# Optimization experiments

Hardware: AMD Instinct MI355X
Metric: run time of the kernel (lower is better)

## Reference

```python
import jax, jax.numpy as jnp
import numpy as np
import math

B, N, C = 8, 2048, 512

def setup_inputs() -> dict:
    key = jax.random.key(0)
    ks = jax.random.split(key, 7)
    s = 1.0 / math.sqrt(C)
    return {
        "feature": jax.random.normal(ks[0], (B, N, C), dtype=jnp.float32),
        "wq": jax.random.uniform(ks[1], (C, C), jnp.float32, -s, s),
        "bq": jax.random.uniform(ks[2], (C,), jnp.float32, -s, s),
        "wk": jax.random.uniform(ks[3], (C, C), jnp.float32, -s, s),
        "bk": jax.random.uniform(ks[4], (C,), jnp.float32, -s, s),
        "wv": jax.random.uniform(ks[5], (C, C), jnp.float32, -s, s),
        "bv": jax.random.uniform(ks[6], (C,), jnp.float32, -s, s),
    }

def reference(feature, wq, bq, wk, bk, wv, bv):
    # torch nn.Linear: x @ W.T + b
    q = jnp.einsum('bnc,dc->bnd', feature, wq) + bq
    k = jnp.einsum('bnc,dc->bnd', feature, wk) + bk
    v = jnp.einsum('bnc,dc->bnd', feature, wv) + bv
    scores = jnp.einsum('bnd,bmd->bnm', q, k)          # [B, N, N]
    attn = jax.nn.softmax(scores, axis=2) / math.sqrt(C)  # post-softmax scale (as in source)
    v_star = jnp.einsum('bnm,bmd->bnd', attn, v)
    return feature + v_star
```

## Files before the change

### kernel.cpp

```cpp
#include <hip/hip_runtime.h>
#include <cstdint>
#include <cstddef>


typedef __bf16 bf16x8 __attribute__((ext_vector_type(8)));
typedef float f32x4 __attribute__((ext_vector_type(4)));
typedef short short4v __attribute__((ext_vector_type(4)));

__device__ __forceinline__ short f2b(float f) {
  union { float f; unsigned u; } u; u.f = f;
  unsigned r = (u.u + 0x7fffu + ((u.u >> 16) & 1u)) >> 16;
  return (short)r;
}

#define GLDS(gptr, lptr) \
  __builtin_amdgcn_global_load_lds( \
      (const __attribute__((address_space(1))) unsigned int*)(const void*)(gptr), \
      (__attribute__((address_space(3))) unsigned int*)(void*)(lptr), 16, 0, 0)

__device__ __forceinline__ bf16x8 ldfrag64(const short* buf, int row, int kq) {
  return *(const bf16x8*)(buf + row * 64 + ((kq ^ (row & 7)) * 8));
}

template <int VM>
__device__ __forceinline__ void ph_mid() {
  if constexpr (VM >= 0) asm volatile("s_waitcnt vmcnt(%0)" ::"n"(VM) : "memory");
  __builtin_amdgcn_s_barrier();
  __builtin_amdgcn_s_setprio(1);
}
__device__ __forceinline__ void ph_end() {
  __builtin_amdgcn_s_setprio(0);
  __builtin_amdgcn_s_barrier();
  __builtin_amdgcn_sched_barrier(0);
}

__device__ __forceinline__ void ldA4(bf16x8 (&a)[4][2], const short* buf, int rb, int l4) {
#pragma unroll
  for (int j = 0; j < 4; ++j)
#pragma unroll
    for (int kk = 0; kk < 2; ++kk) a[j][kk] = ldfrag64(buf, rb + j * 16, kk * 4 + l4);
}
__device__ __forceinline__ void ld2(bf16x8 (&b)[2][2], const short* buf, int rb, int l4) {
#pragma unroll
  for (int n = 0; n < 2; ++n)
#pragma unroll
    for (int kk = 0; kk < 2; ++kk) b[n][kk] = ldfrag64(buf, rb + n * 16, kk * 4 + l4);
}
__device__ __forceinline__ void mm42(f32x4 (&acc)[8][4], const bf16x8 (&a)[4][2],
                                     const bf16x8 (&b)[2][2], int io, int no) {
#pragma unroll
  for (int j = 0; j < 4; ++j)
#pragma unroll
    for (int n = 0; n < 2; ++n)
#pragma unroll
      for (int kk = 0; kk < 2; ++kk)
        acc[io + j][no + n] = __builtin_amdgcn_mfma_f32_16x16x32_bf16(
            a[j][kk], b[n][kk], acc[io + j][no + n], 0, 0, 0);
}
__device__ __forceinline__ void mm22(f32x4 (&acc)[4][4], const bf16x8 (&a)[2][2],
                                     const bf16x8 (&b)[2][2], int io, int no) {
#pragma unroll
  for (int j = 0; j < 2; ++j)
#pragma unroll
    for (int n = 0; n < 2; ++n)
#pragma unroll
      for (int kk = 0; kk < 2; ++kk)
        acc[io + j][no + n] = __builtin_amdgcn_mfma_f32_16x16x32_bf16(
            a[j][kk], b[n][kk], acc[io + j][no + n], 0, 0, 0);
}

__global__ __launch_bounds__(256) void prep(const float* __restrict__ f,
                                            const float* __restrict__ w0,
                                            const float* __restrict__ w1,
                                            const float* __restrict__ w2,
                                            const float* __restrict__ b0,
                                            const float* __restrict__ b1,
                                            const float* __restrict__ b2,
                                            short* __restrict__ Xb, short* __restrict__ Wb,
                                            float* __restrict__ biasP, float* __restrict__ l) {
  const int bid = blockIdx.x;
  const int t = threadIdx.x;
  if (bid < 8192) {
    int i = bid * 256 + t;
    float4 v = ((const float4*)f)[i];
    short4v o = { f2b(v.x), f2b(v.y), f2b(v.z), f2b(v.w) };
    *(short4v*)(Xb + (size_t)i * 4) = o;
  } else if (bid < 8960) {
    int i = (bid - 8192) * 256 + t;
    const float* src = (i < 65536) ? w0 : (i < 131072) ? w1 : w2;
    float4 v = ((const float4*)src)[i & 65535];
    short4v o = { f2b(v.x), f2b(v.y), f2b(v.z), f2b(v.w) };
    *(short4v*)(Wb + (size_t)i * 4) = o;
  } else {
    int i = (bid - 8960) * 256 + t;
    float4 z = { 0.f, 0.f, 0.f, 0.f };
    ((float4*)l)[i * 2] = z;
    ((float4*)l)[i * 2 + 1] = z;
    if (i < 1536) {
      const float* s = (i < 512) ? b0 : (i < 1024) ? b1 : b2;
      biasP[i] = s[i & 511];
    }
  }
}

__global__ __launch_bounds__(256) void gemm_qkv(const short* __restrict__ X,
                                                const short* __restrict__ Wall,
                                                const float* __restrict__ biasP,
                                                short* __restrict__ Out,
                                                short* __restrict__ VtOut) {
  __shared__ __align__(16) short Xs[128 * 64];
  __shared__ __align__(16) short Ws[128 * 64];
  const int z = blockIdx.z;
  const short* Wm = Wall + (size_t)z * 262144;
  const int m0 = blockIdx.y * 128, n0 = blockIdx.x * 128;
  const int t = threadIdx.x;
  const int lane = t & 63, w = t >> 6;
  const int wn = (w & 1) * 64, wm = (w >> 1) * 64;
  const int fr = lane & 15, l4 = lane >> 4;

  f32x4 acc[4][4] = {};

  for (int k0 = 0; k0 < 512; k0 += 64) {
    __syncthreads();
#pragma unroll
    for (int u = 0; u < 4; ++u) {
      int cc = t + u * 256;
      int r = cc >> 3, cs = cc & 7;
      int kk = ((cs ^ (r & 7)) * 8);
      GLDS(X + (size_t)(m0 + r) * 512 + k0 + kk, Xs + cc * 8);
      GLDS(Wm + (size_t)(n0 + r) * 512 + k0 + kk, Ws + cc * 8);
    }
    __syncthreads();
#pragma unroll
    for (int h = 0; h < 2; ++h) {
      bf16x8 wf[4], xf[4];
#pragma unroll
      for (int i = 0; i < 4; ++i) wf[i] = ldfrag64(Ws, wn + i * 16 + fr, h * 4 + l4);
#pragma unroll
      for (int j = 0; j < 4; ++j) xf[j] = ldfrag64(Xs, wm + j * 16 + fr, h * 4 + l4);
      if (z < 2) {
#pragma unroll
        for (int i = 0; i < 4; ++i)
#pragma unroll
          for (int j = 0; j < 4; ++j)
            acc[i][j] = __builtin_amdgcn_mfma_f32_16x16x32_bf16(wf[i], xf[j], acc[i][j], 0, 0, 0);
      } else {
#pragma unroll
        for (int i = 0; i < 4; ++i)
#pragma unroll
          for (int j = 0; j < 4; ++j)
            acc[i][j] = __builtin_amdgcn_mfma_f32_16x16x32_bf16(xf[i], wf[j], acc[i][j], 0, 0, 0);
      }
    }
  }

  const int rq = l4 * 4;
  if (z < 2) {
#pragma unroll
    for (int i = 0; i < 4; ++i) {
      int nb = n0 + wn + i * 16 + rq;
      float4 bs = *(const float4*)(biasP + z * 512 + nb);
#pragma unroll
      for (int j = 0; j < 4; ++j) {
        int m = m0 + wm + j * 16 + fr;
        short4v o = { f2b(acc[i][j][0] + bs.x), f2b(acc[i][j][1] + bs.y),
                      f2b(acc[i][j][2] + bs.z), f2b(acc[i][j][3] + bs.w) };
        *(short4v*)(Out + (size_t)z * 8388608 + (size_t)m * 512 + nb) = o;
      }
    }
  } else {
    const int zB = blockIdx.y >> 4;
    const int mb = m0 & 2047;
#pragma unroll
    for (int j = 0; j < 4; ++j) {
      int d = n0 + wn + j * 16 + fr;
      float bd = biasP[1024 + d];
#pragma unroll
      for (int i = 0; i < 4; ++i) {
        int mloc = mb + wm + i * 16 + rq;
        short4v o = { f2b(acc[i][j][0] + bd), f2b(acc[i][j][1] + bd),
                      f2b(acc[i][j][2] + bd), f2b(acc[i][j][3] + bd) };
        *(short4v*)(VtOut + (size_t)zB * 1048576 + (size_t)d * 2048 + mloc) = o;
      }
    }
  }
}

__global__ __launch_bounds__(512, 2) void gemm_qk8(const short* __restrict__ Q,
                                                   const short* __restrict__ Kb,
                                                   short* __restrict__ P,
                                                   float* __restrict__ l) {
  __shared__ __align__(16) short As[2][16384];
  __shared__ __align__(16) short Bs[2][16384];
  const int z = blockIdx.z;
  const short* __restrict__ A = Kb + (size_t)z * 1048576;
  const short* __restrict__ B = Q + (size_t)z * 1048576;
  const int m0 = blockIdx.y * 256;
  const int n0 = blockIdx.x * 256;
  const int t = threadIdx.x;
  const int lane = t & 63, w = t >> 6;
  const int aw = (w >> 2) * 64, bw = (w & 3) * 32;
  const int fr = lane & 15, l4 = lane >> 4;
  const int r0 = t >> 3;
  const int kswz = ((t & 7) ^ (r0 & 7)) * 8;
  const short* pA = A + (size_t)(m0 + r0) * 512 + kswz;
  const short* pB = B + (size_t)(n0 + r0) * 512 + kswz;

#define QK_STG_A(buf, h, kt) do { \
    GLDS(pA + (size_t)((h) * 128) * 512 + (kt) * 64, &As[(buf)][(h) * 8192 + t * 8]); \
    GLDS(pA + (size_t)((h) * 128 + 64) * 512 + (kt) * 64, &As[(buf)][(h) * 8192 + 4096 + t * 8]); \
  } while (0)
#define QK_STG_B(buf, h, kt) do { \
    GLDS(pB + (size_t)((h) * 128) * 512 + (kt) * 64, &Bs[(buf)][(h) * 8192 + t * 8]); \
    GLDS(pB + (size_t)((h) * 128 + 64) * 512 + (kt) * 64, &Bs[(buf)][(h) * 8192 + 4096 + t * 8]); \
  } while (0)

  f32x4 acc[8][4] = {};

  QK_STG_A(0, 0, 0); QK_STG_B(0, 0, 0); QK_STG_B(0, 1, 0); QK_STG_A(0, 1, 0);
  QK_STG_A(1, 0, 1); QK_STG_B(1, 0, 1); QK_STG_B(1, 1, 1);
  asm volatile("s_waitcnt vmcnt(10)" ::: "memory");
  __builtin_amdgcn_s_barrier();
  __builtin_amdgcn_sched_barrier(0);

  bf16x8 af[4][2], b0[2][2], b1[2][2];
  for (int kt = 0; kt < 6; ++kt) {
    const int c = kt & 1;
    const short* Ac = &As[c][0];
    const short* Bc = &Bs[c][0];
    ldA4(af, Ac, aw + fr, l4); ld2(b0, Bc, bw + fr, l4);
    QK_STG_A(c ^ 1, 1, kt + 1);
    ph_mid<10>(); mm42(acc, af, b0, 0, 0); ph_end();
    ld2(b1, Bc, 128 + bw + fr, l4);
    QK_STG_A(c, 0, kt + 2);
    ph_mid<10>(); mm42(acc, af, b1, 0, 2); ph_end();
    ldA4(af, Ac, 128 + aw + fr, l4);
    QK_STG_B(c, 0, kt + 2);
    ph_mid<-1>(); mm42(acc, af, b1, 4, 2); ph_end();
    QK_STG_B(c, 1, kt + 2);
    ph_mid<10>(); mm42(acc, af, b0, 4, 0); ph_end();
  }
  {
    const short *Ac = &As[0][0], *Bc = &Bs[0][0];
    ldA4(af, Ac, aw + fr, l4); ld2(b0, Bc, bw + fr, l4);
    QK_STG_A(1, 1, 7);
    ph_mid<10>(); mm42(acc, af, b0, 0, 0); ph_end();
    ld2(b1, Bc, 128 + bw + fr, l4);
    ph_mid<8>();  mm42(acc, af, b1, 0, 2); ph_end();
    ldA4(af, Ac, 128 + aw + fr, l4);
    ph_mid<-1>(); mm42(acc, af, b1, 4, 2); ph_end();
    ph_mid<4>();  mm42(acc, af, b0, 4, 0); ph_end();
  }
  {
    const short *Ac = &As[1][0], *Bc = &Bs[1][0];
    ldA4(af, Ac, aw + fr, l4); ld2(b0, Bc, bw + fr, l4);
    ph_mid<2>();  mm42(acc, af, b0, 0, 0); ph_end();
    ld2(b1, Bc, 128 + bw + fr, l4);
    ph_mid<0>();  mm42(acc, af, b1, 0, 2); ph_end();
    ldA4(af, Ac, 128 + aw + fr, l4);
    ph_mid<-1>(); mm42(acc, af, b1, 4, 2); ph_end();
    ph_mid<-1>(); mm42(acc, af, b0, 4, 0); ph_end();
  }
#undef QK_STG_A
#undef QK_STG_B

  const float LOG2E = 1.4426950408889634f;
  float rs[4] = { 0.f, 0.f, 0.f, 0.f };
#pragma unroll
  for (int i = 0; i < 8; ++i) {
    const int key = m0 + aw + (i & 3) * 16 + (i >> 2) * 128 + l4 * 4;
#pragma unroll
    for (int n = 0; n < 4; ++n) {
      const int q = n0 + bw + (n & 1) * 16 + (n >> 1) * 128 + fr;
      short4v o;
      float part = 0.f;
#pragma unroll
      for (int r = 0; r < 4; ++r) {
        float e = exp2f(acc[i][n][r] * LOG2E);
        o[r] = f2b(e);
        part += e;
      }
      *(short4v*)(P + (size_t)z * 4194304 + (size_t)q * 2048 + key) = o;
      rs[n] += part;
    }
  }
#pragma unroll
  for (int n = 0; n < 4; ++n) {
    rs[n] += __shfl_xor(rs[n], 16);
    rs[n] += __shfl_xor(rs[n], 32);
  }
  if (l4 == 0) {
#pragma unroll
    for (int n = 0; n < 4; ++n)
      atomicAdd(&l[z * 2048 + n0 + bw + (n & 1) * 16 + (n >> 1) * 128 + fr], rs[n]);
  }
}

__global__ __launch_bounds__(512, 2) void gemm_pv8(const short* __restrict__ Pm,
                                                   const short* __restrict__ Vt,
                                                   const float* __restrict__ l,
                                                   const float* __restrict__ resid,
                                                   float* __restrict__ out, float scale) {
  __shared__ __align__(16) short As[2][8192];
  __shared__ __align__(16) short Bs[2][16384];
  const int z = blockIdx.z;
  const short* __restrict__ A = Vt + (size_t)z * 1048576;
  const short* __restrict__ B = Pm + (size_t)z * 4194304;
  const int d0 = blockIdx.x * 128;
  const int n0 = blockIdx.y * 256;
  const int t = threadIdx.x;
  const int lane = t & 63, w = t >> 6;
  const int aw = (w >> 2) * 32, bw = (w & 3) * 32;
  const int fr = lane & 15, l4 = lane >> 4;
  const int r0 = t >> 3;
  const int kswz = ((t & 7) ^ (r0 & 7)) * 8;
  const short* pA = A + (size_t)(d0 + r0) * 2048 + kswz;
  const short* pB = B + (size_t)(n0 + r0) * 2048 + kswz;

#define PV_STG_A(buf, h, kt) \
    GLDS(pA + (size_t)((h) * 64) * 2048 + (kt) * 64, &As[(buf)][(h) * 4096 + t * 8])
#define PV_STG_B(buf, h, kt) do { \
    GLDS(pB + (size_t)((h) * 128) * 2048 + (kt) * 64, &Bs[(buf)][(h) * 8192 + t * 8]); \
    GLDS(pB + (size_t)((h) * 128 + 64) * 2048 + (kt) * 64, &Bs[(buf)][(h) * 8192 + 4096 + t * 8]); \
  } while (0)

  f32x4 acc[4][4] = {};

  PV_STG_A(0, 0, 0); PV_STG_B(0, 0, 0); PV_STG_B(0, 1, 0); PV_STG_A(0, 1, 0);
  PV_STG_A(1, 0, 1); PV_STG_B(1, 0, 1); PV_STG_B(1, 1, 1);
  asm volatile("s_waitcnt vmcnt(8)" ::: "memory");
  __builtin_amdgcn_s_barrier();
  __builtin_amdgcn_sched_barrier(0);

  bf16x8 a[2][2], b0[2][2], b1[2][2];
  for (int kt = 0; kt < 30; ++kt) {
    const int c = kt & 1;
    const short* Ac = &As[c][0];
    const short* Bc = &Bs[c][0];
    ld2(a, Ac, aw + fr, l4); ld2(b0, Bc, bw + fr, l4);
    PV_STG_A(c ^ 1, 1, kt + 1);
    ph_mid<7>(); mm22(acc, a, b0, 0, 0); ph_end();
    ld2(b1, Bc, 128 + bw + fr, l4);
    PV_STG_A(c, 0, kt + 2);
    ph_mid<7>(); mm22(acc, a, b1, 0, 2); ph_end();
    ld2(a, Ac, 64 + aw + fr, l4);
    PV_STG_B(c, 0, kt + 2);
    ph_mid<-1>(); mm22(acc, a, b1, 2, 2); ph_end();
    PV_STG_B(c, 1, kt + 2);
    ph_mid<8>(); mm22(acc, a, b0, 2, 0); ph_end();
  }
  {
    const short *Ac = &As[0][0], *Bc = &Bs[0][0];
    ld2(a, Ac, aw + fr, l4); ld2(b0, Bc, bw + fr, l4);
    PV_STG_A(1, 1, 31);
    ph_mid<7>(); mm22(acc, a, b0, 0, 0); ph_end();
    ld2(b1, Bc, 128 + bw + fr, l4);
    ph_mid<6>(); mm22(acc, a, b1, 0, 2); ph_end();
    ld2(a, Ac, 64 + aw + fr, l4);
    ph_mid<-1>(); mm22(acc, a, b1, 2, 2); ph_end();
    ph_mid<3>(); mm22(acc, a, b0, 2, 0); ph_end();
  }
  {
    const short *Ac = &As[1][0], *Bc = &Bs[1][0];
    ld2(a, Ac, aw + fr, l4); ld2(b0, Bc, bw + fr, l4);
    ph_mid<1>(); mm22(acc, a, b0, 0, 0); ph_end();
    ld2(b1, Bc, 128 + bw + fr, l4);
    ph_mid<0>(); mm22(acc, a, b1, 0, 2); ph_end();
    ld2(a, Ac, 64 + aw + fr, l4);
    ph_mid<-1>(); mm22(acc, a, b1, 2, 2); ph_end();
    ph_mid<-1>(); mm22(acc, a, b0, 2, 0); ph_end();
  }
#undef PV_STG_A
#undef PV_STG_B

  float linv[4];
#pragma unroll
  for (int n = 0; n < 4; ++n) {
    const int q = n0 + bw + (n & 1) * 16 + (n >> 1) * 128 + fr;
    linv[n] = scale / l[z * 2048 + q];
  }
#pragma unroll
  for (int n = 0; n < 4; ++n) {
    const int q = n0 + bw + (n & 1) * 16 + (n >> 1) * 128 + fr;
#pragma unroll
    for (int i = 0; i < 4; ++i) {
      const int d = d0 + aw + (i & 1) * 16 + (i >> 1) * 64 + l4 * 4;
      const size_t idx = (size_t)z * 1048576 + (size_t)q * 512 + d;
      float4 rv = *(const float4*)(resid + idx);
      float4 o = { rv.x + acc[i][n][0] * linv[n], rv.y + acc[i][n][1] * linv[n],
                   rv.z + acc[i][n][2] * linv[n], rv.w + acc[i][n][3] * linv[n] };
      *(float4*)(out + idx) = o;
    }
  }
}

extern "C" void kernel_launch(void* const* d_in, const int* in_sizes, int n_in,
                              void* d_out, int out_size, void* d_ws, size_t ws_size,
                              hipStream_t stream) {
  const float* feature = (const float*)d_in[0];
  const float* wq = (const float*)d_in[1];
  const float* bq = (const float*)d_in[2];
  const float* wk = (const float*)d_in[3];
  const float* bk = (const float*)d_in[4];
  const float* wv = (const float*)d_in[5];
  const float* bv = (const float*)d_in[6];
  float* out = (float*)d_out;

  const size_t MN = (size_t)16384 * 512;
  short* Xb = (short*)d_ws;
  short* Wb = Xb + MN;
  short* Q = Wb + 786432;
  short* K = Q + MN;
  short* Vt = K + MN;
  short* P = Vt + MN;
  float* biasP = (float*)(P + (size_t)8 * 2048 * 2048);
  float* l = biasP + 1536;

  prep<<<8968, 256, 0, stream>>>(feature, wq, wk, wv, bq, bk, bv, Xb, Wb, biasP, l);

  gemm_qkv<<<dim3(4, 128, 3), 256, 0, stream>>>(Xb, Wb, biasP, Q, Vt);
  gemm_qk8<<<dim3(8, 8, 8), 512, 0, stream>>>(Q, K, P, l);

  const float iscl = 0.044194173824159216f;
  gemm_pv8<<<dim3(4, 8, 8), 512, 0, stream>>>(P, Vt, l, feature, out, iscl);
}
```

Baseline: 250.5 us.

## Rework GEMM pipeline sync, add inline-asm LDS reads, and swizzle block order

LDS fragment loads become inline-asm ds_read_b128 paired with explicit lgkmcnt(0) waits. The per-phase vmcnt waits are replaced by fewer waits at the end of each k-iteration, and the PV kernel merges its four phases into two so each barrier covers more MFMA work. MFMA loop order puts kk outermost. Both GEMMs also remap the block index so that consecutive workgroups spread across batches and tiles, aiming at better cache or channel locality. The risks are that the hand-counted vmcnt values may no longer cover every global-to-LDS load and that asm loads limit compiler scheduling.

```diff
diff --git a/kernel.cpp b/kernel.cpp
--- a/kernel.cpp
+++ b/kernel.cpp
@@ -22,49 +22,54 @@
   return *(const bf16x8*)(buf + row * 64 + ((kq ^ (row & 7)) * 8));
 }
 
-template <int VM>
-__device__ __forceinline__ void ph_mid() {
-  if constexpr (VM >= 0) asm volatile("s_waitcnt vmcnt(%0)" ::"n"(VM) : "memory");
-  __builtin_amdgcn_s_barrier();
-  __builtin_amdgcn_s_setprio(1);
-}
-__device__ __forceinline__ void ph_end() {
-  __builtin_amdgcn_s_setprio(0);
-  __builtin_amdgcn_s_barrier();
-  __builtin_amdgcn_sched_barrier(0);
-}
+__device__ __forceinline__ bf16x8 ldfrag_a(const short* buf, int row, int kq) {
+  const short* p = buf + row * 64 + ((kq ^ (row & 7)) * 8);
+  bf16x8 r;
+  asm volatile("ds_read_b128 %0, %1"
+               : "=v"(r)
+               : "v"((const __attribute__((address_space(3))) short*)(const void*)p));
+  return r;
+}
+
+#define LGKM0_SB() do { \
+    asm volatile("s_waitcnt lgkmcnt(0)" ::: "memory"); \
+    __builtin_amdgcn_sched_barrier(0); } while (0)
+#define VMW(n) asm volatile("s_waitcnt vmcnt(" #n ")" ::: "memory")
+#define SBAR() __builtin_amdgcn_s_barrier()
+#define PRIO1() __builtin_amdgcn_s_setprio(1)
+#define PRIO0() __builtin_amdgcn_s_setprio(0)
 
 __device__ __forceinline__ void ldA4(bf16x8 (&a)[4][2], const short* buf, int rb, int l4) {
 #pragma unroll
   for (int j = 0; j < 4; ++j)
 #pragma unroll
-    for (int kk = 0; kk < 2; ++kk) a[j][kk] = ldfrag64(buf, rb + j * 16, kk * 4 + l4);
+    for (int kk = 0; kk < 2; ++kk) a[j][kk] = ldfrag_a(buf, rb + j * 16, kk * 4 + l4);
 }
 __device__ __forceinline__ void ld2(bf16x8 (&b)[2][2], const short* buf, int rb, int l4) {
 #pragma unroll
   for (int n = 0; n < 2; ++n)
 #pragma unroll
-    for (int kk = 0; kk < 2; ++kk) b[n][kk] = ldfrag64(buf, rb + n * 16, kk * 4 + l4);
+    for (int kk = 0; kk < 2; ++kk) b[n][kk] = ldfrag_a(buf, rb + n * 16, kk * 4 + l4);
 }
 __device__ __forceinline__ void mm42(f32x4 (&acc)[8][4], const bf16x8 (&a)[4][2],
                                      const bf16x8 (&b)[2][2], int io, int no) {
 #pragma unroll
-  for (int j = 0; j < 4; ++j)
-#pragma unroll
-    for (int n = 0; n < 2; ++n)
-#pragma unroll
-      for (int kk = 0; kk < 2; ++kk)
+  for (int kk = 0; kk < 2; ++kk)
+#pragma unroll
+    for (int j = 0; j < 4; ++j)
+#pragma unroll
+      for (int n = 0; n < 2; ++n)
         acc[io + j][no + n] = __builtin_amdgcn_mfma_f32_16x16x32_bf16(
             a[j][kk], b[n][kk], acc[io + j][no + n], 0, 0, 0);
 }
 __device__ __forceinline__ void mm22(f32x4 (&acc)[4][4], const bf16x8 (&a)[2][2],
                                      const bf16x8 (&b)[2][2], int io, int no) {
 #pragma unroll
-  for (int j = 0; j < 2; ++j)
-#pragma unroll
-    for (int n = 0; n < 2; ++n)
-#pragma unroll
-      for (int kk = 0; kk < 2; ++kk)
+  for (int kk = 0; kk < 2; ++kk)
+#pragma unroll
+    for (int j = 0; j < 2; ++j)
+#pragma unroll
+      for (int n = 0; n < 2; ++n)
         acc[io + j][no + n] = __builtin_amdgcn_mfma_f32_16x16x32_bf16(
             a[j][kk], b[n][kk], acc[io + j][no + n], 0, 0, 0);
 }
@@ -192,11 +197,13 @@
                                                    float* __restrict__ l) {
   __shared__ __align__(16) short As[2][16384];
   __shared__ __align__(16) short Bs[2][16384];
-  const int z = blockIdx.z;
+  const int id = blockIdx.x + blockIdx.y * 8 + blockIdx.z * 64;
+  const int swz = (id & 7) * 64 + (id >> 3);
+  const int z = swz >> 6;
+  const int m0 = ((swz >> 3) & 7) * 256;
+  const int n0 = (swz & 7) * 256;
   const short* __restrict__ A = Kb + (size_t)z * 1048576;
   const short* __restrict__ B = Q + (size_t)z * 1048576;
-  const int m0 = blockIdx.y * 256;
-  const int n0 = blockIdx.x * 256;
   const int t = threadIdx.x;
   const int lane = t & 63, w = t >> 6;
   const int aw = (w >> 2) * 64, bw = (w & 3) * 32;
@@ -219,9 +226,8 @@
 
   QK_STG_A(0, 0, 0); QK_STG_B(0, 0, 0); QK_STG_B(0, 1, 0); QK_STG_A(0, 1, 0);
   QK_STG_A(1, 0, 1); QK_STG_B(1, 0, 1); QK_STG_B(1, 1, 1);
-  asm volatile("s_waitcnt vmcnt(10)" ::: "memory");
-  __builtin_amdgcn_s_barrier();
-  __builtin_amdgcn_sched_barrier(0);
+  VMW(6);
+  SBAR();
 
   bf16x8 af[4][2], b0[2][2], b1[2][2];
   for (int kt = 0; kt < 6; ++kt) {
@@ -230,36 +236,38 @@
     const short* Bc = &Bs[c][0];
     ldA4(af, Ac, aw + fr, l4); ld2(b0, Bc, bw + fr, l4);
     QK_STG_A(c ^ 1, 1, kt + 1);
-    ph_mid<10>(); mm42(acc, af, b0, 0, 0); ph_end();
+    SBAR(); LGKM0_SB(); PRIO1(); mm42(acc, af, b0, 0, 0); PRIO0(); SBAR();
     ld2(b1, Bc, 128 + bw + fr, l4);
     QK_STG_A(c, 0, kt + 2);
-    ph_mid<10>(); mm42(acc, af, b1, 0, 2); ph_end();
+    SBAR(); LGKM0_SB(); PRIO1(); mm42(acc, af, b1, 0, 2); PRIO0(); SBAR();
     ldA4(af, Ac, 128 + aw + fr, l4);
     QK_STG_B(c, 0, kt + 2);
-    ph_mid<-1>(); mm42(acc, af, b1, 4, 2); ph_end();
+    SBAR(); LGKM0_SB(); PRIO1(); mm42(acc, af, b1, 4, 2); PRIO0(); SBAR();
     QK_STG_B(c, 1, kt + 2);
-    ph_mid<10>(); mm42(acc, af, b0, 4, 0); ph_end();
+    VMW(6);
+    SBAR(); PRIO1(); mm42(acc, af, b0, 4, 0); PRIO0(); SBAR();
   }
   {
     const short *Ac = &As[0][0], *Bc = &Bs[0][0];
     ldA4(af, Ac, aw + fr, l4); ld2(b0, Bc, bw + fr, l4);
     QK_STG_A(1, 1, 7);
-    ph_mid<10>(); mm42(acc, af, b0, 0, 0); ph_end();
+    SBAR(); LGKM0_SB(); PRIO1(); mm42(acc, af, b0, 0, 0); PRIO0(); SBAR();
     ld2(b1, Bc, 128 + bw + fr, l4);
-    ph_mid<8>();  mm42(acc, af, b1, 0, 2); ph_end();
+    SBAR(); LGKM0_SB(); PRIO1(); mm42(acc, af, b1, 0, 2); PRIO0(); SBAR();
     ldA4(af, Ac, 128 + aw + fr, l4);
-    ph_mid<-1>(); mm42(acc, af, b1, 4, 2); ph_end();
-    ph_mid<4>();  mm42(acc, af, b0, 4, 0); ph_end();
+    SBAR(); LGKM0_SB(); PRIO1(); mm42(acc, af, b1, 4, 2); PRIO0(); SBAR();
+    VMW(0);
+    SBAR(); PRIO1(); mm42(acc, af, b0, 4, 0); PRIO0(); SBAR();
   }
   {
     const short *Ac = &As[1][0], *Bc = &Bs[1][0];
     ldA4(af, Ac, aw + fr, l4); ld2(b0, Bc, bw + fr, l4);
-    ph_mid<2>();  mm42(acc, af, b0, 0, 0); ph_end();
+    SBAR(); LGKM0_SB(); PRIO1(); mm42(acc, af, b0, 0, 0); PRIO0(); SBAR();
     ld2(b1, Bc, 128 + bw + fr, l4);
-    ph_mid<0>();  mm42(acc, af, b1, 0, 2); ph_end();
+    SBAR(); LGKM0_SB(); PRIO1(); mm42(acc, af, b1, 0, 2); PRIO0(); SBAR();
     ldA4(af, Ac, 128 + aw + fr, l4);
-    ph_mid<-1>(); mm42(acc, af, b1, 4, 2); ph_end();
-    ph_mid<-1>(); mm42(acc, af, b0, 4, 0); ph_end();
+    SBAR(); LGKM0_SB(); PRIO1(); mm42(acc, af, b1, 4, 2); PRIO0();
+    mm42(acc, af, b0, 4, 0);
   }
 #undef QK_STG_A
 #undef QK_STG_B
@@ -303,11 +311,13 @@
                                                    float* __restrict__ out, float scale) {
   __shared__ __align__(16) short As[2][8192];
   __shared__ __align__(16) short Bs[2][16384];
-  const int z = blockIdx.z;
+  const int id = blockIdx.x + blockIdx.y * 4 + blockIdx.z * 32;
+  const int swz = (id & 7) * 32 + (id >> 3);
+  const int z = swz >> 5;
+  const int d0 = (swz & 3) * 128;
+  const int n0 = ((swz >> 2) & 7) * 256;
   const short* __restrict__ A = Vt + (size_t)z * 1048576;
   const short* __restrict__ B = Pm + (size_t)z * 4194304;
-  const int d0 = blockIdx.x * 128;
-  const int n0 = blockIdx.y * 256;
   const int t = threadIdx.x;
   const int lane = t & 63, w = t >> 6;
   const int aw = (w >> 2) * 32, bw = (w & 3) * 32;
@@ -328,47 +338,51 @@
 
   PV_STG_A(0, 0, 0); PV_STG_B(0, 0, 0); PV_STG_B(0, 1, 0); PV_STG_A(0, 1, 0);
   PV_STG_A(1, 0, 1); PV_STG_B(1, 0, 1); PV_STG_B(1, 1, 1);
-  asm volatile("s_waitcnt vmcnt(8)" ::: "memory");
-  __builtin_amdgcn_s_barrier();
-  __builtin_amdgcn_sched_barrier(0);
+  VMW(5);
+  SBAR();
 
   bf16x8 a[2][2], b0[2][2], b1[2][2];
   for (int kt = 0; kt < 30; ++kt) {
     const int c = kt & 1;
     const short* Ac = &As[c][0];
     const short* Bc = &Bs[c][0];
-    ld2(a, Ac, aw + fr, l4); ld2(b0, Bc, bw + fr, l4);
+    ld2(a, Ac, aw + fr, l4); ld2(b0, Bc, bw + fr, l4); ld2(b1, Bc, 128 + bw + fr, l4);
     PV_STG_A(c ^ 1, 1, kt + 1);
-    ph_mid<7>(); mm22(acc, a, b0, 0, 0); ph_end();
-    ld2(b1, Bc, 128 + bw + fr, l4);
+    SBAR(); LGKM0_SB(); PRIO1();
+    mm22(acc, a, b0, 0, 0); mm22(acc, a, b1, 0, 2);
+    PRIO0(); SBAR();
+    ld2(a, Ac, 64 + aw + fr, l4);
     PV_STG_A(c, 0, kt + 2);
-    ph_mid<7>(); mm22(acc, a, b1, 0, 2); ph_end();
-    ld2(a, Ac, 64 + aw + fr, l4);
     PV_STG_B(c, 0, kt + 2);
-    ph_mid<-1>(); mm22(acc, a, b1, 2, 2); ph_end();
     PV_STG_B(c, 1, kt + 2);
-    ph_mid<8>(); mm22(acc, a, b0, 2, 0); ph_end();
+    VMW(5);
+    SBAR(); LGKM0_SB(); PRIO1();
+    mm22(acc, a, b1, 2, 2); mm22(acc, a, b0, 2, 0);
+    PRIO0(); SBAR();
   }
   {
     const short *Ac = &As[0][0], *Bc = &Bs[0][0];
-    ld2(a, Ac, aw + fr, l4); ld2(b0, Bc, bw + fr, l4);
+    ld2(a, Ac, aw + fr, l4); ld2(b0, Bc, bw + fr, l4); ld2(b1, Bc, 128 + bw + fr, l4);
     PV_STG_A(1, 1, 31);
-    ph_mid<7>(); mm22(acc, a, b0, 0, 0); ph_end();
-    ld2(b1, Bc, 128 + bw + fr, l4);
-    ph_mid<6>(); mm22(acc, a, b1, 0, 2); ph_end();
+    SBAR(); LGKM0_SB(); PRIO1();
+    mm22(acc, a, b0, 0, 0); mm22(acc, a, b1, 0, 2);
+    PRIO0(); SBAR();
     ld2(a, Ac, 64 + aw + fr, l4);
-    ph_mid<-1>(); mm22(acc, a, b1, 2, 2); ph_end();
-    ph_mid<3>(); mm22(acc, a, b0, 2, 0); ph_end();
+    VMW(0);
+    SBAR(); LGKM0_SB(); PRIO1();
+    mm22(acc, a, b1, 2, 2); mm22(acc, a, b0, 2, 0);
+    PRIO0(); SBAR();
   }
   {
     const short *Ac = &As[1][0], *Bc = &Bs[1][0];
-    ld2(a, Ac, aw + fr, l4); ld2(b0, Bc, bw + fr, l4);
-    ph_mid<1>(); mm22(acc, a, b0, 0, 0); ph_end();
-    ld2(b1, Bc, 128 + bw + fr, l4);
-    ph_mid<0>(); mm22(acc, a, b1, 0, 2); ph_end();
+    ld2(a, Ac, aw + fr, l4); ld2(b0, Bc, bw + fr, l4); ld2(b1, Bc, 128 + bw + fr, l4);
+    SBAR(); LGKM0_SB(); PRIO1();
+    mm22(acc, a, b0, 0, 0); mm22(acc, a, b1, 0, 2);
+    PRIO0(); SBAR();
     ld2(a, Ac, 64 + aw + fr, l4);
-    ph_mid<-1>(); mm22(acc, a, b1, 2, 2); ph_end();
-    ph_mid<-1>(); mm22(acc, a, b0, 2, 0); ph_end();
+    LGKM0_SB(); PRIO1();
+    mm22(acc, a, b1, 2, 2); mm22(acc, a, b0, 2, 0);
+    PRIO0();
   }
 #undef PV_STG_A
 #undef PV_STG_B
```

Measured after the change: 229.9 us. -8.2%, faster.
